# Kernel optimization log

Hardware: AMD Instinct MI355X
Metric: run time of the kernel (lower is better)

The kernel has to match this reference:

```python
import jax, jax.numpy as jnp
import numpy as np

B, N_IN, D, K, N = 8, 256, 128, 1024, 4096
EMA_GAMMA = 0.99


def setup_inputs() -> dict:
    key = jax.random.key(0)
    k1, k2, k3 = jax.random.split(key, 3)
    z = jax.random.normal(k1, (B, N_IN, N), dtype=jnp.float32)
    # Conv1d(n_in, d, 1, bias=False) == a (d, n_in) matmul; xavier-ish scale
    W_lin = jax.random.normal(k2, (D, N_IN), dtype=jnp.float32) * (1.0 / np.sqrt(N_IN))
    # codebook initialized xavier_uniform with gain=10 in the original
    lim = 10.0 * np.sqrt(6.0 / (K + D))
    emb = jax.random.uniform(k3, (K, D), dtype=jnp.float32, minval=-lim, maxval=lim)
    ema_numer = emb * (1.0 - EMA_GAMMA)
    ema_denom = jnp.ones((K,), dtype=jnp.float32) * (1.0 - EMA_GAMMA)
    return {"z": z, "W_lin": W_lin, "emb": emb,
            "ema_numer": ema_numer, "ema_denom": ema_denom}


def reference(z, W_lin, emb, ema_numer, ema_denom):
    # ze: (B, d, N) -- 1x1 conv == channel matmul
    ze = jnp.einsum('bcn,dc->bdn', z, W_lin)
    sg_emb = jax.lax.stop_gradient(emb)           # codebook is stop-gradded

    # scaled L2 distance:  ||ze - q|| / (||ze|| + ||q||), shape (B, K, N)
    ze_sq = jnp.sum(ze * ze, axis=1)              # (B, N)
    q_sq = jnp.sum(sg_emb * sg_emb, axis=1)       # (K,)
    dots = jnp.einsum('bdn,kd->bkn', ze, sg_emb)  # (B, K, N)
    dist_sq = jnp.maximum(ze_sq[:, None, :] + q_sq[None, :, None] - 2.0 * dots, 0.0)
    den = jnp.sqrt(ze_sq)[:, None, :] + jnp.sqrt(q_sq)[None, :, None]
    snorm = jnp.sqrt(dist_sq) / den               # (B, K, N)

    min_ind = jnp.argmin(snorm, axis=1)           # (B, N) int
    zq = jnp.moveaxis(sg_emb[min_ind], -1, 1)     # (B, d, N)

    # ReplaceGrad: forward value = zq, gradient routed to ze (straight-through)
    zq_rg = ze + jax.lax.stop_gradient(zq - ze)

    # EMA codebook statistics (scatter-add over codebook indices)
    flat_ind = min_ind.reshape(-1)                             # (B*N,)
    ze_flat = jax.lax.stop_gradient(
        jnp.moveaxis(ze, 1, 2).reshape(-1, ze.shape[1]))       # (B*N, d)
    z_sum = jax.ops.segment_sum(ze_flat, flat_ind, num_segments=K)   # (K, d)
    n_sum = jax.ops.segment_sum(jnp.ones(flat_ind.shape, ze.dtype),
                                flat_ind, num_segments=K)            # (K,)
    ema_numer_new = EMA_GAMMA * ema_numer + (1.0 - EMA_GAMMA) * z_sum
    ema_denom_new = EMA_GAMMA * ema_denom + (1.0 - EMA_GAMMA) * n_sum
    return zq_rg, ema_numer_new, ema_denom_new
```

## Files before the change

### kernel.cpp

```cpp
#include <hip/hip_runtime.h>
#include <cmath>
#include <stdint.h>

#define B_    8
#define NIN_  256
#define D_    128
#define K_    1024
#define N_    4096
#define P_    (B_ * N_)
#define MARGIN_M 1e-4f

typedef __attribute__((ext_vector_type(8))) short bf16x8;
typedef __attribute__((ext_vector_type(4))) float f32x4;

#define WS_ZSUM   0
#define WS_CNT    524288
#define WS_FLAGC  528384
#define WS_MEMSET 532480
#define WS_OFF    532480
#define WS_QSQ    536576
#define WS_QNORM  540672
#define WS_KSTAR  544768
#define WS_RANK   675840
#define WS_PLIST  806912
#define WS_KLIST  937984
#define WS_FLIST  1069056
#define WS_WT     1200128
#define WS_ZPM    1331200
#define WS_ZESQ   18108416
#define WS_ZEN    18239488
#define WS_ZE2F   18370560
#define WS_EMB2F  43536384
#define WS_VAL1   44322816
#define WS_IDX1   46419968
#define WS_VAL2   48517120

__device__ inline unsigned short f2bf(float v) {
  union { float f; uint32_t u; } c; c.f = v;
  return (unsigned short)((c.u + 0x7FFFu + ((c.u >> 16) & 1u)) >> 16);
}
__device__ inline float bf2f(unsigned short b) {
  union { float f; uint32_t u; } c; c.u = ((uint32_t)b) << 16; return c.f;
}
__device__ inline uint32_t pack2(float a, float b, int lo) {
  unsigned short ha = f2bf(a); if (lo) ha = f2bf(a - bf2f(ha));
  unsigned short hb = f2bf(b); if (lo) hb = f2bf(b - bf2f(hb));
  return (uint32_t)ha | ((uint32_t)hb << 16);
}

__device__ inline void gl_lds(const uint4* g, uint4* l) {
  __builtin_amdgcn_global_load_lds(
      (const __attribute__((address_space(1))) unsigned int*)g,
      (__attribute__((address_space(3))) unsigned int*)l, 16, 0, 0);
}

__global__ __launch_bounds__(256) void prep_kernel(
    const float* __restrict__ W, const float* __restrict__ emb,
    float* __restrict__ Wt, float* __restrict__ q_sq, float* __restrict__ q_norm,
    uint4* __restrict__ emb2f, uint4* __restrict__ wszero)
{
  const int tid = threadIdx.x;
  const int bid = blockIdx.x;
  if (bid < 128) {
    int t = bid * 256 + tid;
    int c = t >> 7, d = t & 127;
    Wt[t] = W[d * NIN_ + c];
  } else if (bid < 132) {
    int k = (bid - 128) * 256 + tid;
    const float* e = emb + (size_t)k * D_;
    float s = 0.f;
    #pragma unroll 8
    for (int d = 0; d < D_; ++d) s = fmaf(e[d], e[d], s);
    q_sq[k] = s;
    q_norm[k] = sqrtf(s);
  } else if (bid < 196) {
    const int kt = bid - 132;
    #pragma unroll
    for (int i = 0; i < 3; ++i) {
      int f    = i * 256 + tid;
      int c    = f >> 6;
      int lane = f & 63;
      int k    = kt * 16 + (lane & 15);
      int q    = lane >> 4;
      int kk0  = c * 32 + q * 8;
      int lo   = (kk0 >> 7) == 1;
      int d0   = kk0 & 127;
      float4 v0 = *(const float4*)&emb[(size_t)k * D_ + d0];
      float4 v1 = *(const float4*)&emb[(size_t)k * D_ + d0 + 4];
      uint4 u;
      u.x = pack2(v0.x, v0.y, lo);
      u.y = pack2(v0.z, v0.w, lo);
      u.z = pack2(v1.x, v1.y, lo);
      u.w = pack2(v1.z, v1.w, lo);
      emb2f[(size_t)kt * 768 + f] = u;
    }
  } else {
    int t = (bid - 196) * 256 + tid;
    wszero[t] = make_uint4(0u, 0u, 0u, 0u);
  }
}

__global__ __launch_bounds__(1024) void ze_kernel(
    const float* __restrict__ z, const float* __restrict__ Wt,
    float* __restrict__ ze_pm, float* __restrict__ ze_sq,
    float* __restrict__ ze_norm, uint4* __restrict__ ze2f)
{
  __shared__ float tile[64][132];
  __shared__ float sqpart[16][64];
  const int t    = threadIdx.x;
  const int lane = t & 63;
  const int wv   = __builtin_amdgcn_readfirstlane(t >> 6);
  const int p    = blockIdx.x * 64 + lane;
  const int b    = p >> 12;
  const int n    = p & (N_ - 1);

  float acc[8];
  #pragma unroll
  for (int j = 0; j < 8; ++j) acc[j] = 0.f;
  const float* zp = z + (size_t)b * NIN_ * N_ + n;
  const float* wp = Wt + wv * 8;
  #pragma unroll 8
  for (int c = 0; c < NIN_; ++c) {
    float zv = zp[(size_t)c * N_];
    #pragma unroll
    for (int j = 0; j < 8; ++j)
      acc[j] = fmaf(wp[c * D_ + j], zv, acc[j]);
  }
  #pragma unroll
  for (int j = 0; j < 8; ++j) tile[lane][wv * 8 + j] = acc[j];
  float s = 0.f;
  #pragma unroll
  for (int j = 0; j < 8; ++j) s = fmaf(acc[j], acc[j], s);
  sqpart[wv][lane] = s;
  __syncthreads();
  if (wv == 0) {
    float tt = sqpart[0][lane];
    #pragma unroll
    for (int w = 1; w < 16; ++w) tt += sqpart[w][lane];
    ze_sq[p] = tt;
    ze_norm[p] = sqrtf(tt);
  }
  const int row = t >> 5;
  const int c4  = (t & 31) * 4;
  #pragma unroll
  for (int r = 0; r < 2; ++r) {
    int pr = r * 32 + row;
    float4 v = *(const float4*)&tile[pr][c4];
    *(float4*)&ze_pm[(size_t)(blockIdx.x * 64 + pr) * D_ + c4] = v;
  }
  #pragma unroll
  for (int i = 0; i < 3; ++i) {
    int f    = i * 1024 + t;
    int lane_f = f & 63;
    int g    = f >> 6;
    int c    = g % 12;
    int lpt  = g / 12;
    int pl   = lpt * 16 + (lane_f & 15);
    int q    = lane_f >> 4;
    int kk0  = c * 32 + q * 8;
    int lo   = (kk0 >> 7) == 2;
    int d0   = kk0 & 127;
    float4 v0 = *(const float4*)&tile[pl][d0];
    float4 v1 = *(const float4*)&tile[pl][d0 + 4];
    uint4 u;
    u.x = pack2(v0.x, v0.y, lo);
    u.y = pack2(v0.z, v0.w, lo);
    u.z = pack2(v1.x, v1.y, lo);
    u.w = pack2(v1.z, v1.w, lo);
    ze2f[((size_t)(blockIdx.x * 4 + lpt) * 12 + c) * 64 + lane_f] = u;
  }
}

__global__ __launch_bounds__(256, 4) void mfma_argmin_kernel(
    const uint4* __restrict__ ze2f, const uint4* __restrict__ emb2f,
    const float* __restrict__ ze_sq, const float* __restrict__ ze_norm,
    const float* __restrict__ q_sq, const float* __restrict__ q_norm,
    float* __restrict__ val1, int* __restrict__ idx1, float* __restrict__ val2)
{
  __shared__ uint4 Ls[2][16][64];
  const int tid  = threadIdx.x;
  const int lane = tid & 63;
  const int w    = __builtin_amdgcn_readfirstlane(tid >> 6);
  const int x    = blockIdx.x & 7;
  const int ib   = blockIdx.x >> 3;
  const int pb3  = x * 32 + (ib & 31);
  const int kb2  = ib >> 5;
  const int pt0  = pb3 * 8;
  const int ct0  = kb2 * 8;
  const int wm   = w >> 1;
  const int wn   = w & 1;
  const int wq   = w * 4;
  const int wm4  = wm * 4;
  const int wn4  = wn * 4;

  const uint4* sbase = (w < 2)
      ? ze2f  + ((size_t)(pt0 + w * 4) * 12) * 64 + lane
      : emb2f + ((size_t)(ct0 + (w - 2) * 4) * 12) * 64 + lane;

  f32x4 acc[4][4];
  #pragma unroll
  for (int ii = 0; ii < 4; ++ii)
    #pragma unroll
    for (int jj = 0; jj < 4; ++jj) acc[ii][jj] = (f32x4){0.f, 0.f, 0.f, 0.f};

#define STAGE(NB, C)                                                        \
  gl_lds(sbase + 0 * 768 + (C) * 64, &Ls[NB][wq + 0][0]);                   \
  gl_lds(sbase + 1 * 768 + (C) * 64, &Ls[NB][wq + 1][0]);                   \
  gl_lds(sbase + 2 * 768 + (C) * 64, &Ls[NB][wq + 2][0]);                   \
  gl_lds(sbase + 3 * 768 + (C) * 64, &Ls[NB][wq + 3][0]);

#define MFMA_STEP(CUR)                                                      \
  {                                                                         \
    uint4 afr[4], bfr[4];                                                   \
    afr[0] = Ls[CUR][wm4 + 0][lane];  afr[1] = Ls[CUR][wm4 + 1][lane];      \
    afr[2] = Ls[CUR][wm4 + 2][lane];  afr[3] = Ls[CUR][wm4 + 3][lane];      \
    bfr[0] = Ls[CUR][8 + wn4 + 0][lane]; bfr[1] = Ls[CUR][8 + wn4 + 1][lane]; \
    bfr[2] = Ls[CUR][8 + wn4 + 2][lane]; bfr[3] = Ls[CUR][8 + wn4 + 3][lane]; \
    __builtin_amdgcn_s_setprio(1);                                          \
    _Pragma("unroll")                                                       \
    for (int ii = 0; ii < 4; ++ii) {                                        \
      union { uint4 u; bf16x8 h; } au; au.u = afr[ii];                      \
      _Pragma("unroll")                                                     \
      for (int jj = 0; jj < 4; ++jj) {                                      \
        union { uint4 u; bf16x8 h; } bu; bu.u = bfr[jj];                    \
        acc[ii][jj] = __builtin_amdgcn_mfma_f32_16x16x32_bf16(au.h, bu.h,   \
                                                        acc[ii][jj], 0, 0, 0); \
      }                                                                     \
    }                                                                       \
    __builtin_amdgcn_s_setprio(0);                                          \
  }

#define STEP_MID(C, CUR, NXT)                                               \
  STAGE(NXT, (C) + 1)                                                       \
  asm volatile("s_waitcnt vmcnt(4)" ::: "memory");                          \
  __builtin_amdgcn_s_barrier();                                             \
  __builtin_amdgcn_sched_barrier(0);                                        \
  MFMA_STEP(CUR)                                                            \
  __builtin_amdgcn_s_barrier();                                             \
  __builtin_amdgcn_sched_barrier(0);

  STAGE(0, 0)
  STEP_MID(0, 0, 1)  STEP_MID(1, 1, 0)  STEP_MID(2, 0, 1)  STEP_MID(3, 1, 0)
  STEP_MID(4, 0, 1)  STEP_MID(5, 1, 0)  STEP_MID(6, 0, 1)  STEP_MID(7, 1, 0)
  STEP_MID(8, 0, 1)  STEP_MID(9, 1, 0)  STEP_MID(10, 0, 1)
  asm volatile("s_waitcnt vmcnt(0)" ::: "memory");
  __builtin_amdgcn_s_barrier();
  __builtin_amdgcn_sched_barrier(0);
  MFMA_STEP(1)

#undef STEP_MID
#undef MFMA_STEP
#undef STAGE

  const int col = lane & 15;
  const int q   = lane >> 4;
  float qsq_l[4], qn_l[4]; int kg[4];
  #pragma unroll
  for (int j = 0; j < 4; ++j) {
    kg[j]    = kb2 * 128 + wn * 64 + j * 16 + col;
    qsq_l[j] = q_sq[kg[j]];
    qn_l[j]  = q_norm[kg[j]];
  }
  const int g = kb2 * 2 + wn;
  #pragma unroll
  for (int ii = 0; ii < 4; ++ii) {
    const int pbase = pb3 * 128 + wm * 64 + ii * 16 + q * 4;
    f32x4 zs = *(const f32x4*)&ze_sq[pbase];
    f32x4 zn = *(const f32x4*)&ze_norm[pbase];
    float m1r[4], m2r[4]; int k1r[4];
    #pragma unroll
    for (int r = 0; r < 4; ++r) { m1r[r] = 1e30f; m2r[r] = 1e30f; k1r[r] = 0; }
    #pragma unroll
    for (int j = 0; j < 4; ++j) {
      #pragma unroll
      for (int r = 0; r < 4; ++r) {
        float dsq = fmaxf(zs[r] + qsq_l[j] - 2.0f * acc[ii][j][r], 0.0f);
        float den = zn[r] + qn_l[j];
        float rd  = __builtin_amdgcn_rcpf(den);
        float m   = dsq * rd * rd;
        bool take = m < m1r[r];
        float loser = take ? m1r[r] : m;
        if (take) { m1r[r] = m; k1r[r] = kg[j]; }
        m2r[r] = fminf(m2r[r], loser);
      }
    }
    #pragma unroll
    for (int ms = 1; ms <= 8; ms <<= 1) {
      #pragma unroll
      for (int r = 0; r < 4; ++r) {
        float om1 = __shfl_xor(m1r[r], ms);
        int   ok1 = __shfl_xor(k1r[r], ms);
        float om2 = __shfl_xor(m2r[r], ms);
        bool take = (om1 < m1r[r]) || (om1 == m1r[r] && ok1 < k1r[r]);
        float loser = take ? m1r[r] : om1;
        if (take) { m1r[r] = om1; k1r[r] = ok1; }
        m2r[r] = fminf(fminf(m2r[r], om2), loser);
      }
    }
    if (col == 0) {
      const size_t o = (size_t)g * P_ + pbase;
      *(float4*)&val1[o] = make_float4(m1r[0], m1r[1], m1r[2], m1r[3]);
      *(int4*)&idx1[o]   = make_int4(k1r[0], k1r[1], k1r[2], k1r[3]);
      *(float4*)&val2[o] = make_float4(m2r[0], m2r[1], m2r[2], m2r[3]);
    }
  }
}

__global__ __launch_bounds__(256) void resolve_kernel(
    const float* __restrict__ val1, const int* __restrict__ idx1,
    const float* __restrict__ val2, int* __restrict__ kstar,
    int* __restrict__ rank, int* __restrict__ counts,
    int* __restrict__ flaglist, int* __restrict__ flagcnt)
{
  const int p = blockIdx.x * 256 + threadIdx.x;
  float m1 = 1e30f, m2 = 1e30f; int k1 = 0;
  #pragma unroll
  for (int g = 0; g < 16; ++g) {
    float v1 = val1[(size_t)g * P_ + p];
    int   i1 = idx1[(size_t)g * P_ + p];
    float v2 = val2[(size_t)g * P_ + p];
    bool take = v1 < m1;
    float loser = take ? m1 : v1;
    if (take) { m1 = v1; k1 = i1; }
    m2 = fminf(fminf(m2, v2), loser);
  }
  kstar[p] = k1;
  if (m2 - m1 <= MARGIN_M) {
    int s = atomicAdd(flagcnt, 1);
    flaglist[s] = p;
  } else {
    rank[p] = atomicAdd(&counts[k1], 1);
  }
}

__global__ __launch_bounds__(256) void fallback_kernel(
    const float* __restrict__ ze_pm, const float* __restrict__ emb,
    const float* __restrict__ ze_sq, const float* __restrict__ ze_norm,
    const float* __restrict__ q_sq, const float* __restrict__ q_norm,
    const int* __restrict__ flaglist, const int* __restrict__ flagcnt,
    int* __restrict__ kstar, int* __restrict__ rank, int* __restrict__ counts)
{
  __shared__ float zlds[128];
  __shared__ float wbs[4];
  __shared__ int   wbk[4];
  const int tid  = threadIdx.x;
  const int lane = tid & 63;
  const int w    = tid >> 6;
  const int cnt  = *flagcnt;
  for (int i = blockIdx.x; i < cnt; i += gridDim.x) {
    const int p = flaglist[i];
    __syncthreads();
    if (tid < 128) zlds[tid] = ze_pm[(size_t)p * D_ + tid];
    __syncthreads();
    const float zsq = ze_sq[p], zn = ze_norm[p];
    float bs = 1e30f; int bk = 0;
    #pragma unroll
    for (int tt = 0; tt < 4; ++tt) {
      const int k = (w * 4 + tt) * 64 + lane;
      const float* e = emb + (size_t)k * D_;
      float dot = 0.f;
      #pragma unroll 8
      for (int d = 0; d < D_; ++d)
        dot = fmaf(zlds[d], e[d], dot);
      float dsq = fmaxf(fmaf(-2.0f, dot, zsq + q_sq[k]), 0.0f);
      float sn  = sqrtf(dsq) / (zn + q_norm[k]);
      if (sn < bs) { bs = sn; bk = k; }
    }
    #pragma unroll
    for (int m = 1; m <= 32; m <<= 1) {
      float ov = __shfl_xor(bs, m);
      int   ok = __shfl_xor(bk, m);
      if (ov < bs || (ov == bs && ok < bk)) { bs = ov; bk = ok; }
    }
    if (lane == 0) { wbs[w] = bs; wbk[w] = bk; }
    __syncthreads();
    if (tid == 0) {
      float fb = wbs[0]; int fk = wbk[0];
      #pragma unroll
      for (int ww = 1; ww < 4; ++ww) {
        if (wbs[ww] < fb) { fb = wbs[ww]; fk = wbk[ww]; }
      }
      kstar[p] = fk;
      rank[p] = atomicAdd(&counts[fk], 1);
    }
  }
}

__global__ __launch_bounds__(1024) void prefix_kernel(
    const int* __restrict__ counts, const float* __restrict__ ema_denom,
    int* __restrict__ offsets, float* __restrict__ out_den)
{
  __shared__ int s[1024];
  const int t = threadIdx.x;
  const int c = counts[t];
  s[t] = c;
  __syncthreads();
  for (int off = 1; off < 1024; off <<= 1) {
    int v = (t >= off) ? s[t - off] : 0;
    __syncthreads();
    s[t] += v;
    __syncthreads();
  }
  offsets[t] = s[t] - c;
  out_den[t] = 0.99f * ema_denom[t] + 0.01f * (float)c;
}

__global__ __launch_bounds__(512) void zq_kernel(
    const float* __restrict__ ze_pm, const float* __restrict__ emb,
    const int* __restrict__ kstar, const int* __restrict__ rank,
    const int* __restrict__ offsets, int* __restrict__ pos_list,
    int* __restrict__ k_list, float* __restrict__ out)
{
  const int tid = threadIdx.x;
  const int lane = tid & 63;
  const int w = __builtin_amdgcn_readfirstlane(tid >> 6);
  const int p = blockIdx.x * 64 + lane;
  const int b = p >> 12;
  const int n = p & (N_ - 1);
  const int kst = kstar[p];

  if (w == 0) {
    const int slot = offsets[kst] + rank[p];
    pos_list[slot] = p;
    k_list[slot] = kst;
  }

  const float* zr = ze_pm + (size_t)p * D_ + w * 16;
  const float* ek = emb + (size_t)kst * D_ + w * 16;
  float* op = out + (size_t)b * D_ * N_ + (size_t)(w * 16) * N_ + n;
  float4 zv[4], ev[4];
  #pragma unroll
  for (int r = 0; r < 4; ++r) {
    zv[r] = *(const float4*)&zr[r * 4];
    ev[r] = *(const float4*)&ek[r * 4];
  }
  #pragma unroll
  for (int r = 0; r < 4; ++r) {
    const float* zc = (const float*)&zv[r];
    const float* ec = (const float*)&ev[r];
    #pragma unroll
    for (int jj = 0; jj < 4; ++jj) {
      float zev = zc[jj];
      op[(size_t)(r * 4 + jj) * N_] = zev + (ec[jj] - zev);
    }
  }
}

__global__ __launch_bounds__(128) void gsum_kernel(
    const float* __restrict__ ze_pm, const int* __restrict__ pos_list,
    const int* __restrict__ k_list, float* __restrict__ z_sum)
{
  const int d  = threadIdx.x;
  const int i0 = blockIdx.x * 32;
  int   kprev = -1;
  float acc = 0.f;
  #pragma unroll
  for (int ii = 0; ii < 32; ++ii) {
    int p = pos_list[i0 + ii];
    int k = k_list[i0 + ii];
    if (k != kprev) {
      if (kprev >= 0) atomicAdd(&z_sum[(size_t)kprev * D_ + d], acc);
      acc = 0.f;
      kprev = k;
    }
    acc += ze_pm[(size_t)p * D_ + d];
  }
  if (kprev >= 0) atomicAdd(&z_sum[(size_t)kprev * D_ + d], acc);
}

__global__ __launch_bounds__(256) void finalize_num_kernel(
    const float* __restrict__ ema_numer, const float* __restrict__ z_sum,
    float* __restrict__ out)
{
  const int t = blockIdx.x * 256 + threadIdx.x;
  float* out_num = out + (size_t)B_ * D_ * N_;
  out_num[t] = 0.99f * ema_numer[t] + 0.01f * z_sum[t];
}

extern "C" void kernel_launch(void* const* d_in, const int* in_sizes, int n_in,
                              void* d_out, int out_size, void* d_ws, size_t ws_size,
                              hipStream_t stream)
{
  (void)in_sizes; (void)n_in; (void)out_size; (void)ws_size;
  const float* z         = (const float*)d_in[0];
  const float* W         = (const float*)d_in[1];
  const float* emb       = (const float*)d_in[2];
  const float* ema_numer = (const float*)d_in[3];
  const float* ema_denom = (const float*)d_in[4];
  float* out = (float*)d_out;
  char*  ws  = (char*)d_ws;
  float* z_sum   = (float*)(ws + WS_ZSUM);
  int*   counts  = (int*)(ws + WS_CNT);
  int*   flagcnt = (int*)(ws + WS_FLAGC);
  int*   offsets = (int*)(ws + WS_OFF);
  float* q_sq    = (float*)(ws + WS_QSQ);
  float* q_norm  = (float*)(ws + WS_QNORM);
  int*   kstar   = (int*)(ws + WS_KSTAR);
  int*   rank    = (int*)(ws + WS_RANK);
  int*   plist   = (int*)(ws + WS_PLIST);
  int*   klist   = (int*)(ws + WS_KLIST);
  int*   flist   = (int*)(ws + WS_FLIST);
  float* Wt      = (float*)(ws + WS_WT);
  float* ze_pm   = (float*)(ws + WS_ZPM);
  float* ze_sq   = (float*)(ws + WS_ZESQ);
  float* ze_norm = (float*)(ws + WS_ZEN);
  uint4* ze2f    = (uint4*)(ws + WS_ZE2F);
  uint4* emb2f   = (uint4*)(ws + WS_EMB2F);
  float* val1    = (float*)(ws + WS_VAL1);
  int*   idx1    = (int*)(ws + WS_IDX1);
  float* val2    = (float*)(ws + WS_VAL2);
  float* out_den = out + (size_t)B_ * D_ * N_ + K_ * D_;

  prep_kernel<<<326, 256, 0, stream>>>(W, emb, Wt, q_sq, q_norm, emb2f,
                                       (uint4*)ws);
  ze_kernel<<<P_ / 64, 1024, 0, stream>>>(z, Wt, ze_pm, ze_sq, ze_norm, ze2f);
  mfma_argmin_kernel<<<2048, 256, 0, stream>>>(ze2f, emb2f, ze_sq, ze_norm,
                                               q_sq, q_norm, val1, idx1, val2);
  resolve_kernel<<<P_ / 256, 256, 0, stream>>>(val1, idx1, val2, kstar,
                                               rank, counts, flist, flagcnt);
  fallback_kernel<<<1024, 256, 0, stream>>>(ze_pm, emb, ze_sq, ze_norm,
                                            q_sq, q_norm, flist, flagcnt,
                                            kstar, rank, counts);
  prefix_kernel<<<1, 1024, 0, stream>>>(counts, ema_denom, offsets, out_den);
  zq_kernel<<<P_ / 64, 512, 0, stream>>>(ze_pm, emb, kstar, rank,
                                         offsets, plist, klist, out);
  gsum_kernel<<<P_ / 32, 128, 0, stream>>>(ze_pm, plist, klist, z_sum);
  finalize_num_kernel<<<K_ * D_ / 256, 256, 0, stream>>>(ema_numer, z_sum, out);
}
```

Measured before the change: 247.0 us.

## Fuse prefix scan into fallback tail and replace atomic gsum with per-code reduction

```diff
diff --git a/kernel.cpp b/kernel.cpp
--- a/kernel.cpp
+++ b/kernel.cpp
@@ -16,7 +16,6 @@
 #define WS_ZSUM   0
 #define WS_CNT    524288
 #define WS_FLAGC  528384
-#define WS_MEMSET 532480
 #define WS_OFF    532480
 #define WS_QSQ    536576
 #define WS_QNORM  540672
@@ -96,7 +95,7 @@
     }
   } else {
     int t = (bid - 196) * 256 + tid;
-    wszero[t] = make_uint4(0u, 0u, 0u, 0u);
+    if (t < 512) wszero[t] = make_uint4(0u, 0u, 0u, 0u);
   }
 }
 
@@ -337,12 +336,16 @@
     const float* __restrict__ ze_pm, const float* __restrict__ emb,
     const float* __restrict__ ze_sq, const float* __restrict__ ze_norm,
     const float* __restrict__ q_sq, const float* __restrict__ q_norm,
-    const int* __restrict__ flaglist, const int* __restrict__ flagcnt,
-    int* __restrict__ kstar, int* __restrict__ rank, int* __restrict__ counts)
+    const int* __restrict__ flaglist, int* __restrict__ flagcnt,
+    int* __restrict__ kstar, int* __restrict__ rank, int* __restrict__ counts,
+    int* __restrict__ offsets, const float* __restrict__ ema_denom,
+    float* __restrict__ out_den)
 {
   __shared__ float zlds[128];
   __shared__ float wbs[4];
   __shared__ int   wbk[4];
+  __shared__ int   lastflag;
+  __shared__ int   part[256];
   const int tid  = threadIdx.x;
   const int lane = tid & 63;
   const int w    = tid >> 6;
@@ -384,25 +387,40 @@
       rank[p] = atomicAdd(&counts[fk], 1);
     }
   }
-}
-
-__global__ __launch_bounds__(1024) void prefix_kernel(
-    const int* __restrict__ counts, const float* __restrict__ ema_denom,
-    int* __restrict__ offsets, float* __restrict__ out_den)
-{
-  __shared__ int s[1024];
-  const int t = threadIdx.x;
-  const int c = counts[t];
-  s[t] = c;
   __syncthreads();
-  for (int off = 1; off < 1024; off <<= 1) {
-    int v = (t >= off) ? s[t - off] : 0;
+  if (tid == 0) {
+    __threadfence();
+    int old = atomicAdd(flagcnt + 1, 1);
+    lastflag = (old == (int)gridDim.x - 1);
+  }
+  __syncthreads();
+  if (lastflag) {
+    __threadfence();
+    int v[4], inc[4];
+    #pragma unroll
+    for (int i2 = 0; i2 < 4; ++i2)
+      v[i2] = __hip_atomic_load(&counts[tid * 4 + i2], __ATOMIC_RELAXED,
+                                __HIP_MEMORY_SCOPE_AGENT);
+    int run = 0;
+    #pragma unroll
+    for (int i2 = 0; i2 < 4; ++i2) { run += v[i2]; inc[i2] = run; }
+    part[tid] = run;
     __syncthreads();
-    s[t] += v;
-    __syncthreads();
-  }
-  offsets[t] = s[t] - c;
-  out_den[t] = 0.99f * ema_denom[t] + 0.01f * (float)c;
+    for (int off = 1; off < 256; off <<= 1) {
+      int add = (tid >= off) ? part[tid - off] : 0;
+      __syncthreads();
+      part[tid] += add;
+      __syncthreads();
+    }
+    const int base = (tid > 0) ? part[tid - 1] : 0;
+    #pragma unroll
+    for (int i2 = 0; i2 < 4; ++i2) {
+      const int idx = tid * 4 + i2;
+      const int incl = base + inc[i2];
+      offsets[idx] = incl - v[i2];
+      out_den[idx] = 0.99f * ema_denom[idx] + 0.01f * (float)v[i2];
+    }
+  }
 }
 
 __global__ __launch_bounds__(512) void zq_kernel(
@@ -446,35 +464,23 @@
   }
 }
 
-__global__ __launch_bounds__(128) void gsum_kernel(
+__global__ __launch_bounds__(128) void ksum_kernel(
     const float* __restrict__ ze_pm, const int* __restrict__ pos_list,
-    const int* __restrict__ k_list, float* __restrict__ z_sum)
-{
+    const int* __restrict__ offsets, const int* __restrict__ counts,
+    const float* __restrict__ ema_numer, float* __restrict__ out_num)
+{
+  const int k  = blockIdx.x;
   const int d  = threadIdx.x;
-  const int i0 = blockIdx.x * 32;
-  int   kprev = -1;
-  float acc = 0.f;
-  #pragma unroll
-  for (int ii = 0; ii < 32; ++ii) {
-    int p = pos_list[i0 + ii];
-    int k = k_list[i0 + ii];
-    if (k != kprev) {
-      if (kprev >= 0) atomicAdd(&z_sum[(size_t)kprev * D_ + d], acc);
-      acc = 0.f;
-      kprev = k;
-    }
-    acc += ze_pm[(size_t)p * D_ + d];
-  }
-  if (kprev >= 0) atomicAdd(&z_sum[(size_t)kprev * D_ + d], acc);
-}
-
-__global__ __launch_bounds__(256) void finalize_num_kernel(
-    const float* __restrict__ ema_numer, const float* __restrict__ z_sum,
-    float* __restrict__ out)
-{
-  const int t = blockIdx.x * 256 + threadIdx.x;
-  float* out_num = out + (size_t)B_ * D_ * N_;
-  out_num[t] = 0.99f * ema_numer[t] + 0.01f * z_sum[t];
+  const int o0 = offsets[k];
+  const int c  = counts[k];
+  float s = 0.f;
+  #pragma unroll 4
+  for (int i = 0; i < c; ++i) {
+    const int p = pos_list[o0 + i];
+    s += ze_pm[(size_t)p * D_ + d];
+  }
+  const int idx = k * D_ + d;
+  out_num[idx] = 0.99f * ema_numer[idx] + 0.01f * s;
 }
 
 extern "C" void kernel_launch(void* const* d_in, const int* in_sizes, int n_in,
@@ -489,7 +495,6 @@
   const float* ema_denom = (const float*)d_in[4];
   float* out = (float*)d_out;
   char*  ws  = (char*)d_ws;
-  float* z_sum   = (float*)(ws + WS_ZSUM);
   int*   counts  = (int*)(ws + WS_CNT);
   int*   flagcnt = (int*)(ws + WS_FLAGC);
   int*   offsets = (int*)(ws + WS_OFF);
@@ -509,10 +514,11 @@
   float* val1    = (float*)(ws + WS_VAL1);
   int*   idx1    = (int*)(ws + WS_IDX1);
   float* val2    = (float*)(ws + WS_VAL2);
+  float* out_num = out + (size_t)B_ * D_ * N_;
   float* out_den = out + (size_t)B_ * D_ * N_ + K_ * D_;
 
-  prep_kernel<<<326, 256, 0, stream>>>(W, emb, Wt, q_sq, q_norm, emb2f,
-                                       (uint4*)ws);
+  prep_kernel<<<198, 256, 0, stream>>>(W, emb, Wt, q_sq, q_norm, emb2f,
+                                       (uint4*)(ws + WS_CNT));
   ze_kernel<<<P_ / 64, 1024, 0, stream>>>(z, Wt, ze_pm, ze_sq, ze_norm, ze2f);
   mfma_argmin_kernel<<<2048, 256, 0, stream>>>(ze2f, emb2f, ze_sq, ze_norm,
                                                q_sq, q_norm, val1, idx1, val2);
@@ -520,10 +526,10 @@
                                                rank, counts, flist, flagcnt);
   fallback_kernel<<<1024, 256, 0, stream>>>(ze_pm, emb, ze_sq, ze_norm,
                                             q_sq, q_norm, flist, flagcnt,
-                                            kstar, rank, counts);
-  prefix_kernel<<<1, 1024, 0, stream>>>(counts, ema_denom, offsets, out_den);
+                                            kstar, rank, counts,
+                                            offsets, ema_denom, out_den);
   zq_kernel<<<P_ / 64, 512, 0, stream>>>(ze_pm, emb, kstar, rank,
                                          offsets, plist, klist, out);
-  gsum_kernel<<<P_ / 32, 128, 0, stream>>>(ze_pm, plist, klist, z_sum);
-  finalize_num_kernel<<<K_ * D_ / 256, 256, 0, stream>>>(ema_numer, z_sum, out);
-}
+  ksum_kernel<<<K_, 128, 0, stream>>>(ze_pm, plist, offsets, counts,
+                                      ema_numer, out_num);
+}
```

Result: slower. 272.7 us (+10.4%).
